# Optimization experiments

Hardware: AMD Instinct MI355X
Metric: run time of the kernel (lower is better)

## Reference

```python
import jax, jax.numpy as jnp
import numpy as np
import math

H = 16          # head_count
D = 1024        # model_dim
DT = 100        # topic_dim
DH = D // H     # dim_per_head


def _lin(x, W, b):
    return x @ W.T + b


def _shape(x, B):
    # [B, L, D] -> [B, H, L, DH]
    return x.reshape(B, -1, H, DH).transpose(0, 2, 1, 3)


def setup_inputs() -> dict:
    key = jax.random.key(0)
    ks = jax.random.split(key, 20)
    B, L = 4, 1024
    s = 0.02
    inp = {
        'key': jax.random.normal(ks[0], (B, L, D), jnp.float32),
        'value': jax.random.normal(ks[1], (B, L, D), jnp.float32),
        'query': jax.random.normal(ks[2], (B, L, D), jnp.float32),
        'mask': jax.random.randint(ks[3], (B, L, L), 0, 2).astype(bool),
        'topic_vec': jax.random.normal(ks[4], (B, L, DT), jnp.float32),
        'Wq': jax.random.normal(ks[5], (D, D), jnp.float32) * s,
        'bq': jnp.zeros((D,), jnp.float32),
        'Wk': jax.random.normal(ks[6], (D, D), jnp.float32) * s,
        'bk': jnp.zeros((D,), jnp.float32),
        'Wv': jax.random.normal(ks[7], (D, D), jnp.float32) * s,
        'bv': jnp.zeros((D,), jnp.float32),
        'Wtk': jax.random.normal(ks[8], (D, D), jnp.float32) * s,
        'btk': jnp.zeros((D,), jnp.float32),
        'Wtv': jax.random.normal(ks[9], (D, DT), jnp.float32) * s,
        'btv': jnp.zeros((D,), jnp.float32),
        'Wtw': jax.random.normal(ks[10], (H, 3 * D), jnp.float32) * s,
        'btw': jnp.zeros((H,), jnp.float32),
        'Wo': jax.random.normal(ks[11], (D, D), jnp.float32) * s,
        'bo': jnp.zeros((D,), jnp.float32),
    }
    return inp


def reference(key, value, query, mask, topic_vec,
              Wq, bq, Wk, bk, Wv, bv, Wtk, btk, Wtv, btv, Wtw, btw, Wo, bo):
    B = key.shape[0]
    # content and topic projections
    q_lin = _lin(query, Wq, bq)          # [B, L, D]
    k_lin = _lin(key, Wk, bk)
    v_lin = _lin(value, Wv, bv)
    tk_lin = _lin(key, Wtk, btk)         # topic keys from key states
    tv_lin = _lin(topic_vec, Wtv, btv)   # topic queries from topic distribution

    q = _shape(q_lin, B) / math.sqrt(DH)   # [B, H, Lq, DH]
    k = _shape(k_lin, B)
    v = _shape(v_lin, B)
    tk = _shape(tk_lin, B)
    tq = _shape(tv_lin, B) / math.sqrt(DH)

    scores = jnp.einsum('bhqd,bhkd->bhqk', q, k)          # content scores
    topic_scores = jnp.einsum('bhqd,bhkd->bhqk', tq, tk)  # topic scores

    # per-query, per-head mixing gate from concatenated projections (3*D -> H)
    gate = jax.nn.sigmoid(_lin(jnp.concatenate([q_lin, tk_lin, tv_lin], axis=-1), Wtw, btw))  # [B, L, H]
    p = gate.transpose(0, 2, 1)[..., None]                # [B, H, Lq, 1]
    scores = (1.0 - p) * scores + p * topic_scores

    # masked_fill(mask, -1e18), mask broadcast over heads
    scores = jnp.where(mask[:, None, :, :], -1e18, scores)
    attn = jax.nn.softmax(scores, axis=-1)
    # dropout is identity at eval time
    ctx = jnp.einsum('bhqk,bhkd->bhqd', attn, v)
    ctx = ctx.transpose(0, 2, 1, 3).reshape(B, -1, D)     # unshape
    return ctx @ Wo.T + bo
```

## Files before the change

kernel.cpp:

```cpp
#include <hip/hip_runtime.h>
#include <hip/hip_bf16.h>

#define BB 4
#define LL 1024
#define DD 1024
#define HH 16
#define DHH 64
#define DTT 100
#define ML (BB*LL)
#define LOG2E 1.4426950408889634f

typedef float f32x4 __attribute__((ext_vector_type(4)));
typedef short s16x8 __attribute__((ext_vector_type(8)));

__device__ __forceinline__ unsigned short f2bf(float x) {
    unsigned u = __builtin_bit_cast(unsigned, x);
    return (unsigned short)((u + 0x7FFFu + ((u >> 16) & 1u)) >> 16);
}
__device__ __forceinline__ unsigned short f2bf_fast(float x) {
    return (unsigned short)((__builtin_bit_cast(unsigned, x) + 0x8000u) >> 16);
}
__device__ __forceinline__ unsigned cvt_pk_bf16(float lo, float hi) {
    unsigned r;
    asm("v_cvt_pk_bf16_f32 %0, %1, %2" : "=v"(r) : "v"(lo), "v"(hi));
    return r;
}
__device__ __forceinline__ float bflo(unsigned u) { return __builtin_bit_cast(float, u << 16); }
__device__ __forceinline__ float bfhi(unsigned u) { return __builtin_bit_cast(float, u & 0xFFFF0000u); }
__device__ __forceinline__ int4 pack_bf16x8(float4 x0, float4 x1) {
    int4 o;
    o.x = cvt_pk_bf16(x0.x, x0.y); o.y = cvt_pk_bf16(x0.z, x0.w);
    o.z = cvt_pk_bf16(x1.x, x1.y); o.w = cvt_pk_bf16(x1.z, x1.w);
    return o;
}
__device__ __forceinline__ void gl_lds16(const unsigned short* g, char* l) {
    __builtin_amdgcn_global_load_lds(
        (const __attribute__((address_space(1))) unsigned*)g,
        (__attribute__((address_space(3))) unsigned*)l, 16, 0, 0);
}
__device__ __forceinline__ void barrier_lgkm() {
    __builtin_amdgcn_sched_barrier(0);
    asm volatile("s_waitcnt lgkmcnt(0)" ::: "memory");
    __builtin_amdgcn_sched_barrier(0);
    __builtin_amdgcn_s_barrier();
    __builtin_amdgcn_sched_barrier(0);
}

__global__ __launch_bounds__(256)
void conv_fused(const float* __restrict__ qf, const float* __restrict__ kf,
                const float* __restrict__ vf,
                unsigned short* __restrict__ qb, unsigned short* __restrict__ kb,
                unsigned short* __restrict__ vb,
                const float* __restrict__ w0, const float* __restrict__ w1,
                const float* __restrict__ w2, const float* __restrict__ w3,
                const float* __restrict__ w4, unsigned short* __restrict__ wd,
                const float* __restrict__ wtw, unsigned short* __restrict__ wtwd,
                const float* __restrict__ wtv, unsigned short* __restrict__ wtvd,
                const float* __restrict__ topic, unsigned short* __restrict__ topicd,
                const int* __restrict__ mask, unsigned long long* __restrict__ MB) {
    const int bx0 = blockIdx.x, tid = threadIdx.x;
    if (bx0 < 6144) {
        const int which = bx0 >> 11;
        const float* src = which == 0 ? qf : (which == 1 ? kf : vf);
        unsigned short* dst = which == 0 ? qb : (which == 1 ? kb : vb);
        const int idx = (bx0 & 2047) * 256 + tid;
        float4 f0 = *(const float4*)(src + (size_t)idx * 8);
        float4 f1 = *(const float4*)(src + (size_t)idx * 8 + 4);
        *(int4*)(dst + (size_t)idx * 8) = pack_bf16x8(f0, f1);
        return;
    }
    const int bx = bx0 - 6144;
    if (bx < 2560) {
        const int which = bx >> 9;
        const float* src;
        switch (which) {
            case 0:  src = w0; break;
            case 1:  src = w1; break;
            case 2:  src = w2; break;
            case 3:  src = w3; break;
            default: src = w4; break;
        }
        unsigned short* dst = wd + (size_t)which * DD * DD;
        const int idx = (bx & 511) * 256 + tid;
        float4 f0 = *(const float4*)(src + (size_t)idx * 8);
        float4 f1 = *(const float4*)(src + (size_t)idx * 8 + 4);
        *(int4*)(dst + (size_t)idx * 8) = pack_bf16x8(f0, f1);
    } else if (bx < 2584) {
        const int idx = (bx - 2560) * 256 + tid;
        float4 f0 = *(const float4*)(wtw + (size_t)idx * 8);
        float4 f1 = *(const float4*)(wtw + (size_t)idx * 8 + 4);
        *(int4*)(wtwd + (size_t)idx * 8) = pack_bf16x8(f0, f1);
    } else if (bx < 2648) {
        const int idx = (bx - 2584) * 256 + tid;
        const int r = idx >> 4, c0 = (idx & 15) * 8;
        unsigned short o[8];
        #pragma unroll
        for (int j = 0; j < 8; j++) {
            int c = c0 + j;
            o[j] = (c < DTT) ? f2bf(wtv[(size_t)r * DTT + c]) : (unsigned short)0;
        }
        int4 v;
        v.x = o[0] | ((unsigned)o[1] << 16);
        v.y = o[2] | ((unsigned)o[3] << 16);
        v.z = o[4] | ((unsigned)o[5] << 16);
        v.w = o[6] | ((unsigned)o[7] << 16);
        *(int4*)(wtvd + (size_t)r * 128 + c0) = v;
    } else if (bx < 2904) {
        const int idx = (bx - 2648) * 256 + tid;
        const int r = idx >> 4, c0 = (idx & 15) * 8;
        unsigned short o[8];
        #pragma unroll
        for (int j = 0; j < 8; j++) {
            int c = c0 + j;
            o[j] = (c < DTT) ? f2bf(topic[(size_t)r * DTT + c]) : (unsigned short)0;
        }
        int4 v;
        v.x = o[0] | ((unsigned)o[1] << 16);
        v.y = o[2] | ((unsigned)o[3] << 16);
        v.z = o[4] | ((unsigned)o[5] << 16);
        v.w = o[6] | ((unsigned)o[7] << 16);
        *(int4*)(topicd + (size_t)r * 128 + c0) = v;
    } else {
        const int ww = (bx - 2904) * 4 + (tid >> 6);
        const int lane = tid & 63;
        int v = mask[(size_t)ww * 64 + lane];
        unsigned long long bits = __ballot(v != 0);
        if (lane == 0) MB[ww] = bits;
    }
}

struct GArg { const void* A; const unsigned short* W; const float* bias; void* C; int mode; };

#define STAGE256(kt_, Ad_, Bd_) { \
    const unsigned short* agp_ = Ag + (size_t)(kt_) * 64; \
    const unsigned short* bgp_ = Bg + (size_t)(kt_) * 64; \
    _Pragma("unroll") \
    for (int i_ = 0; i_ < 4; i_++) { \
        gl_lds16(agp_ + (size_t)(i_ * 64) * K, (Ad_) + i_ * 8192 + ldst); \
        gl_lds16(bgp_ + (size_t)(i_ * 64) * K, (Bd_) + i_ * 8192 + ldst); \
    } }

__global__ __launch_bounds__(512, 2)
void gemm256(GArg a0, GArg a1, GArg a2, GArg a3, int N, int K) {
    __shared__ char lds[131072];

    const int nb = gridDim.x * gridDim.y * gridDim.z;
    const int flat = blockIdx.x + gridDim.x * (blockIdx.y + gridDim.y * blockIdx.z);
    const int wid = (flat & 7) * (nb >> 3) + (flat >> 3);
    const int bx = wid % gridDim.x;
    const int rem = wid / gridDim.x;
    const int by = rem % gridDim.y;
    const int bz = rem / gridDim.y;

    GArg a;
    switch (bz) {
        case 0:  a = a0; break;
        case 1:  a = a1; break;
        case 2:  a = a2; break;
        default: a = a3; break;
    }

    const int tid = threadIdx.x, w = tid >> 6, l = tid & 63;
    const int g = l >> 4, c = l & 15;
    const int wm = w >> 2, wn = w & 3;
    const int bm = by * 256, bn = bx * 256;
    const int NK = K >> 6;

    const int srow = tid >> 3;
    const int scol = (tid & 7) ^ (srow & 7);
    const unsigned short* const Ag = (const unsigned short*)a.A + (size_t)(bm + srow) * K + scol * 8;
    const unsigned short* const Bg = a.W + (size_t)(bn + srow) * K + scol * 8;
    const int ldst = tid * 16;

    f32x4 acc[8][4];
    #pragma unroll
    for (int m = 0; m < 8; m++)
        #pragma unroll
        for (int n = 0; n < 4; n++)
            #pragma unroll
            for (int j = 0; j < 4; j++) acc[m][n][j] = 0.f;

    STAGE256(0, lds, lds + 32768)
    if (NK > 1) STAGE256(1, lds + 65536, lds + 98304)

    for (int kt = 0; kt < NK; kt++) {
        char* Ab = lds + (kt & 1) * 65536;
        char* Bb = Ab + 32768;
        if (kt + 1 < NK) { asm volatile("s_waitcnt vmcnt(8)" ::: "memory"); }
        else             { asm volatile("s_waitcnt vmcnt(0)" ::: "memory"); }
        __builtin_amdgcn_sched_barrier(0);
        __builtin_amdgcn_s_barrier();
        __builtin_amdgcn_sched_barrier(0);

        s16x8 bfr[4][2];
        #pragma unroll
        for (int n = 0; n < 4; n++) {
            const int rb = wn * 64 + n * 16 + c;
            #pragma unroll
            for (int ks = 0; ks < 2; ks++)
                bfr[n][ks] = *(const s16x8*)(Bb + rb * 128 + (((ks * 4 + g) ^ (rb & 7)) << 4));
        }
        s16x8 a0[8];
        #pragma unroll
        for (int m = 0; m < 8; m++) {
            const int ra = wm * 128 + m * 16 + c;
            a0[m] = *(const s16x8*)(Ab + ra * 128 + ((g ^ (ra & 7)) << 4));
        }
        #pragma unroll
        for (int m = 0; m < 8; m++)
            #pragma unroll
            for (int n = 0; n < 4; n++)
                acc[m][n] = __builtin_amdgcn_mfma_f32_16x16x32_bf16(a0[m], bfr[n][0], acc[m][n], 0, 0, 0);
        s16x8 a1[8];
        #pragma unroll
        for (int m = 0; m < 8; m++) {
            const int ra = wm * 128 + m * 16 + c;
            a1[m] = *(const s16x8*)(Ab + ra * 128 + (((4 + g) ^ (ra & 7)) << 4));
        }
        barrier_lgkm();
        if (kt + 2 < NK) STAGE256(kt + 2, Ab, Bb)
        #pragma unroll
        for (int m = 0; m < 8; m++)
            #pragma unroll
            for (int n = 0; n < 4; n++)
                acc[m][n] = __builtin_amdgcn_mfma_f32_16x16x32_bf16(a1[m], bfr[n][1], acc[m][n], 0, 0, 0);
    }

    const int mode = a.mode;
    if (mode == 1) {
        unsigned short* C = (unsigned short*)a.C;
        #pragma unroll
        for (int n = 0; n < 4; n++) {
            const int col = bn + wn * 64 + n * 16 + c;
            const float bv = a.bias[col];
            #pragma unroll
            for (int m = 0; m < 8; m++) {
                const int row = bm + wm * 128 + m * 16 + g * 4;
                #pragma unroll
                for (int j = 0; j < 4; j++)
                    C[(size_t)(row + j) * N + col] = f2bf(acc[m][n][j] + bv);
            }
        }
    } else if (mode == 2 || mode == 3) {
        unsigned short* C = (unsigned short*)a.C;
        const int off = (mode == 2) ? 0 : 64;
        #pragma unroll
        for (int n = 0; n < 4; n++) {
            const int col = bn + wn * 64 + n * 16 + c;
            const float bv = a.bias[col];
            const int h = col >> 6, d = col & 63;
            #pragma unroll
            for (int m = 0; m < 8; m++) {
                const int row = bm + wm * 128 + m * 16 + g * 4;
                #pragma unroll
                for (int j = 0; j < 4; j++) {
                    const int rr = row + j;
                    C[((size_t)((rr >> 10) * HH + h) * LL + (rr & 1023)) * 128 + off + d] =
                        f2bf(acc[m][n][j] + bv);
                }
            }
        }
    } else {
        unsigned short* C = (unsigned short*)a.C;
        #pragma unroll
        for (int n = 0; n < 4; n++) {
            const int col = bn + wn * 64 + n * 16 + c;
            const float bv = a.bias[col];
            const int h = col >> 6, d = col & 63;
            #pragma unroll
            for (int m = 0; m < 8; m++) {
                const int row = bm + wm * 128 + m * 16 + g * 4;
                unsigned lo = cvt_pk_bf16(acc[m][n][0] + bv, acc[m][n][1] + bv);
                unsigned hi = cvt_pk_bf16(acc[m][n][2] + bv, acc[m][n][3] + bv);
                unsigned long long pk = (unsigned long long)lo | ((unsigned long long)hi << 32);
                *(unsigned long long*)(C + ((size_t)((row >> 10) * HH + h) * 64 + d) * LL + (row & 1023)) = pk;
            }
        }
    }
}

#define LOADW(s0_,s1_,s2_,s3_,kk) \
    s0_ = *(const int4*)(Wb + (kk)); \
    s1_ = *(const int4*)(Wb + (kk) + wstep); \
    s2_ = *(const int4*)(Wb + (kk) + 2 * wstep); \
    s3_ = *(const int4*)(Wb + (kk) + 3 * wstep);
#define STOREW(s0_,s1_,s2_,s3_) \
    *(int4*)(bsl)         = s0_; \
    *(int4*)(bsl + 4096)  = s1_; \
    *(int4*)(bsl + 8192)  = s2_; \
    *(int4*)(bsl + 12288) = s3_;
#define LOADA16(s0_,s1_,s2_,s3_,kk) \
    s0_ = *(const int4*)(Ab16 + (kk)); \
    s1_ = *(const int4*)(Ab16 + (kk) + wstep); \
    s2_ = *(const int4*)(Ab16 + (kk) + 2 * wstep); \
    s3_ = *(const int4*)(Ab16 + (kk) + 3 * wstep);
#define STOREA16(s0_,s1_,s2_,s3_) \
    *(int4*)(asl)         = s0_; \
    *(int4*)(asl + 4096)  = s1_; \
    *(int4*)(asl + 8192)  = s2_; \
    *(int4*)(asl + 12288) = s3_;
#define GEMM_COMPUTE(ABASE, BBASE) \
    _Pragma("unroll") \
    for (int ks = 0; ks < 2; ks++) { \
        s16x8 af[4], bf[4]; \
        _Pragma("unroll") \
        for (int m = 0; m < 4; m++) { \
            const int ra = wr * 64 + m * 16 + c; \
            af[m] = *(const s16x8*)((ABASE) + ra * 128 + (((ks * 4 + g) ^ (ra & 7)) << 4)); \
            const int rb = wc * 64 + m * 16 + c; \
            bf[m] = *(const s16x8*)((BBASE) + rb * 128 + (((ks * 4 + g) ^ (rb & 7)) << 4)); \
        } \
        _Pragma("unroll") \
        for (int m = 0; m < 4; m++) \
            _Pragma("unroll") \
            for (int n = 0; n < 4; n++) \
                acc[m][n] = __builtin_amdgcn_mfma_f32_16x16x32_bf16(af[m], bf[n], acc[m][n], 0, 0, 0); \
    }

__global__ __launch_bounds__(256, 3)
void gemm_mfma(GArg a0, GArg a1, GArg a2, GArg a3, int N, int K) {
    __shared__ char lds[32768];
    char* As = lds;
    char* Bs = lds + 16384;

    const int nb = gridDim.x * gridDim.y * gridDim.z;
    const int flat = blockIdx.x + gridDim.x * (blockIdx.y + gridDim.y * blockIdx.z);
    const int wid = (flat & 7) * (nb >> 3) + (flat >> 3);
    const int bx = wid % gridDim.x;
    const int rem = wid / gridDim.x;
    const int by = rem % gridDim.y;
    const int bz = rem / gridDim.y;

    GArg a;
    switch (bz) {
        case 0:  a = a0; break;
        case 1:  a = a1; break;
        case 2:  a = a2; break;
        default: a = a3; break;
    }

    const int tid = threadIdx.x, w = tid >> 6, l = tid & 63;
    const int g = l >> 4, c = l & 15;
    const int wr = w >> 1, wc = w & 1;
    const int bm = by * 128, bn = bx * 128;

    const int r0 = tid >> 3, sl = tid & 7;
    char* const asl = As + r0 * 128 + ((sl ^ (r0 & 7)) << 4);
    char* const bsl = Bs + r0 * 128 + ((sl ^ (r0 & 7)) << 4);
    const size_t wstep = (size_t)32 * K;
    const unsigned short* const Wb   = a.W + (size_t)(bn + r0) * K + sl * 8;
    const unsigned short* const Ab16 = (const unsigned short*)a.A + (size_t)(bm + r0) * K + sl * 8;

    f32x4 acc[4][4];
    #pragma unroll
    for (int m = 0; m < 4; m++)
        #pragma unroll
        for (int n = 0; n < 4; n++)
            #pragma unroll
            for (int j = 0; j < 4; j++) acc[m][n][j] = 0.f;

    int4 pw0, pw1, pw2, pw3;
    int4 pa0, pa1, pa2, pa3;
    LOADW(pw0, pw1, pw2, pw3, 0)
    LOADA16(pa0, pa1, pa2, pa3, 0)

    for (int k0 = 0; k0 < K; k0 += 64) {
        barrier_lgkm();
        STOREA16(pa0, pa1, pa2, pa3)
        STOREW(pw0, pw1, pw2, pw3)
        {
            const int kn = (k0 + 64 < K) ? (k0 + 64) : 0;
            LOADW(pw0, pw1, pw2, pw3, kn)
            LOADA16(pa0, pa1, pa2, pa3, kn)
        }
        barrier_lgkm();
        GEMM_COMPUTE(As, Bs)
    }

    const int mode = a.mode;
    if (mode == 0) {
        float* C = (float*)a.C;
        #pragma unroll
        for (int n = 0; n < 4; n++) {
            const int col = bn + wc * 64 + n * 16 + c;
            const float bv = a.bias[col];
            #pragma unroll
            for (int m = 0; m < 4; m++) {
                const int row = bm + wr * 64 + m * 16 + g * 4;
                #pragma unroll
                for (int j = 0; j < 4; j++)
                    C[(size_t)(row + j) * N + col] = acc[m][n][j] + bv;
            }
        }
    } else {
        unsigned short* C = (unsigned short*)a.C;
        #pragma unroll
        for (int n = 0; n < 4; n++) {
            const int col = bn + wc * 64 + n * 16 + c;
            const float bv = a.bias[col];
            #pragma unroll
            for (int m = 0; m < 4; m++) {
                const int row = bm + wr * 64 + m * 16 + g * 4;
                #pragma unroll
                for (int j = 0; j < 4; j++)
                    C[(size_t)(row + j) * N + col] = f2bf(acc[m][n][j] + bv);
            }
        }
    }
}

__global__ __launch_bounds__(256)
void gate_kernel(const unsigned short* __restrict__ QLb,
                 const unsigned short* __restrict__ KCb,
                 const unsigned short* __restrict__ TVLb,
                 const unsigned short* __restrict__ Wtwb,
                 const float* __restrict__ btw, float* __restrict__ GATE) {
    const int t = threadIdx.x;
    const int q = t >> 6, sub = t & 63, row = sub >> 4, h = sub & 15;
    const int row_g = blockIdx.x * 4 + row;
    const int b = row_g >> 10, l = row_g & 1023;

    float acc = 0.f;
    const unsigned short* wp = Wtwb + h * 3 * DD + q * 768;
    #pragma unroll 4
    for (int cc = 0; cc < 96; cc++) {
        const int i = q * 768 + cc * 8;
        const unsigned short* xp;
        if (i < 1024) {
            xp = QLb + (size_t)row_g * DD + i;
        } else if (i < 2048) {
            const int j = i - 1024;
            xp = KCb + ((size_t)(b * HH + (j >> 6)) * LL + l) * 128 + 64 + (j & 63);
        } else {
            xp = TVLb + (size_t)row_g * DD + (i - 2048);
        }
        int4 xv = *(const int4*)xp;
        int4 wv = *(const int4*)(wp + cc * 8);
        const unsigned xs[4] = {(unsigned)xv.x, (unsigned)xv.y, (unsigned)xv.z, (unsigned)xv.w};
        const unsigned ws[4] = {(unsigned)wv.x, (unsigned)wv.y, (unsigned)wv.z, (unsigned)wv.w};
        #pragma unroll
        for (int jj = 0; jj < 4; jj++) {
            acc = fmaf(bflo(xs[jj]), bflo(ws[jj]), acc);
            acc = fmaf(bfhi(xs[jj]), bfhi(ws[jj]), acc);
        }
    }
    __shared__ float part[4][4][16];
    part[q][row][h] = acc;
    __syncthreads();
    if (t < 64) {
        float s = part[0][row][h] + part[1][row][h] + part[2][row][h] + part[3][row][h] + btw[h];
        GATE[(size_t)row_g * HH + h] = 1.f / (1.f + __expf(-s));
    }
}

__global__ __launch_bounds__(256, 3)
void attn_mfma(const unsigned short* __restrict__ QLb,
               const unsigned short* __restrict__ TVLb,
               const float* __restrict__ GATE,
               const unsigned short* __restrict__ KC,
               const unsigned short* __restrict__ VT,
               const unsigned long long* __restrict__ MB,
               unsigned short* __restrict__ CTb) {
    __shared__ char lds[32768];
    char* kc_l = lds;
    char* vt_l = lds + 16384;
    char* p_l  = lds + 24576;

    const int tid = threadIdx.x, w = tid >> 6, l = tid & 63;
    const int g = l >> 4, c = l & 15;
    const int flat = blockIdx.y * gridDim.x + blockIdx.x;
    const int wid = (flat & 7) * 128 + (flat >> 3);
    const int qb = wid & 15, bh = wid >> 4;
    const int b = bh >> 4, h = bh & 15;
    const int q0 = qb * 64;

    const size_t kcg = (size_t)bh * LL * 128;
    const size_t vtg = (size_t)bh * 64 * LL;

    const int kr = tid >> 4, ks = tid & 15;
    const size_t kgo = (size_t)kr * 128 + ks * 8;
    char* const klb = kc_l + kr * 256 + ((ks ^ (kr & 7)) << 4);
    const int vr = tid >> 3, vs = tid & 7;
    const size_t vgo = (size_t)vr * LL + vs * 8;
    char* const vlb = vt_l + vr * 128 + ((vs ^ (vr & 7)) << 4);

    int4 pk0, pk1, pk2, pk3, pv0, pv1;
    {
        const unsigned short* kp = KC + kcg + kgo;
        pk0 = *(const int4*)kp;
        pk1 = *(const int4*)(kp + 16 * 128);
        pk2 = *(const int4*)(kp + 32 * 128);
        pk3 = *(const int4*)(kp + 48 * 128);
        const unsigned short* vp = VT + vtg + vgo;
        pv0 = *(const int4*)vp;
        pv1 = *(const int4*)(vp + 32 * LL);
    }

    {
        const size_t rowbase = (size_t)b * LL + q0 + kr;
        const unsigned short* qsrc =
            (ks < 8 ? QLb : TVLb) + rowbase * DD + h * DHH + (ks & 7) * 8;
        const float* gp = GATE + rowbase * HH + h;
        #pragma unroll
        for (int i = 0; i < 4; i++) {
            const float p = gp[(size_t)i * 16 * HH];
            const float sc = (ks < 8 ? 1.f - p : p) * (0.125f * LOG2E);
            int4 v = *(const int4*)(qsrc + (size_t)i * 16 * DD);
            int4 o;
            o.x = cvt_pk_bf16(bflo((unsigned)v.x) * sc, bfhi((unsigned)v.x) * sc);
            o.y = cvt_pk_bf16(bflo((unsigned)v.y) * sc, bfhi((unsigned)v.y) * sc);
            o.z = cvt_pk_bf16(bflo((unsigned)v.z) * sc, bfhi((unsigned)v.z) * sc);
            o.w = cvt_pk_bf16(bflo((unsigned)v.w) * sc, bfhi((unsigned)v.w) * sc);
            *(int4*)(klb + i * 4096) = o;
        }
    }
    barrier_lgkm();
    s16x8 qf[4];
    const int ql = w * 16 + c;
    #pragma unroll
    for (int kss = 0; kss < 4; kss++) {
        int t = kss * 4 + g;
        qf[kss] = *(s16x8*)(kc_l + ql * 256 + ((t ^ (ql & 7)) << 4));
    }

    f32x4 ctx[4], la;
    #pragma unroll
    for (int ct = 0; ct < 4; ct++)
        #pragma unroll
        for (int j = 0; j < 4; j++) ctx[ct][j] = 0.f;
    #pragma unroll
    for (int j = 0; j < 4; j++) la[j] = 0.f;
    float m_s = -1e18f;

    s16x8 ones;
    #pragma unroll
    for (int j = 0; j < 8; j++) ones[j] = (short)0x3F80;

    const unsigned long long* mbq = MB + ((size_t)b * LL + q0 + w * 16 + c) * 16;
    unsigned long long mw_cur = mbq[0];

    for (int kt = 0; kt < 16; kt++) {
        barrier_lgkm();
        *(int4*)(klb)          = pk0;
        *(int4*)(klb + 4096)   = pk1;
        *(int4*)(klb + 8192)   = pk2;
        *(int4*)(klb + 12288)  = pk3;
        *(int4*)(vlb)          = pv0;
        *(int4*)(vlb + 4096)   = pv1;
        unsigned long long mw_nxt;
        {
            const unsigned short* kp = KC + kcg + (size_t)(kt + 1) * (64 * 128) + kgo;
            pk0 = *(const int4*)kp;
            pk1 = *(const int4*)(kp + 16 * 128);
            pk2 = *(const int4*)(kp + 32 * 128);
            pk3 = *(const int4*)(kp + 48 * 128);
            const unsigned short* vp = VT + vtg + (size_t)(kt + 1) * 64 + vgo;
            pv0 = *(const int4*)vp;
            pv1 = *(const int4*)(vp + 32 * LL);
            mw_nxt = mbq[kt + 1 < 16 ? kt + 1 : 15];
        }
        barrier_lgkm();

        f32x4 sf[4];
        #pragma unroll
        for (int ct = 0; ct < 4; ct++) {
            f32x4 acc;
            #pragma unroll
            for (int j = 0; j < 4; j++) acc[j] = 0.f;
            const int rk = ct * 16 + c;
            #pragma unroll
            for (int kss = 0; kss < 4; kss++) {
                int t = kss * 4 + g;
                s16x8 kf = *(s16x8*)(kc_l + rk * 256 + ((t ^ (rk & 7)) << 4));
                acc = __builtin_amdgcn_mfma_f32_16x16x32_bf16(kf, qf[kss], acc, 0, 0, 0);
            }
            sf[ct] = acc;
        }

        {
            const unsigned long long mw = mw_cur;
            mw_cur = mw_nxt;
            const unsigned ms0 = (unsigned)(mw >> (g * 4));
            const unsigned ms1 = (unsigned)(mw >> (g * 4 + 32));
            #pragma unroll
            for (int ct = 0; ct < 4; ct++) {
                const unsigned mm = (ct & 2) ? ms1 : ms0;
                const int sh = (ct & 1) ? 16 : 0;
                #pragma unroll
                for (int j = 0; j < 4; j++)
                    if ((mm >> (sh + j)) & 1u) sf[ct][j] = -1e18f;
            }
            float t0 = fmaxf(fmaxf(sf[0][0], sf[0][1]), fmaxf(sf[0][2], sf[0][3]));
            float t1 = fmaxf(fmaxf(sf[1][0], sf[1][1]), fmaxf(sf[1][2], sf[1][3]));
            float t2 = fmaxf(fmaxf(sf[2][0], sf[2][1]), fmaxf(sf[2][2], sf[2][3]));
            float t3 = fmaxf(fmaxf(sf[3][0], sf[3][1]), fmaxf(sf[3][2], sf[3][3]));
            float mx = fmaxf(fmaxf(t0, t1), fmaxf(t2, t3));
            mx = fmaxf(mx, __shfl_xor(mx, 16));
            mx = fmaxf(mx, __shfl_xor(mx, 32));
            const float mn = fmaxf(m_s, mx);
            const float cf = exp2f(m_s - mn);
            m_s = mn;

            const float cr0 = __shfl(cf, g * 4 + 0, 16);
            const float cr1 = __shfl(cf, g * 4 + 1, 16);
            const float cr2 = __shfl(cf, g * 4 + 2, 16);
            const float cr3 = __shfl(cf, g * 4 + 3, 16);
            #pragma unroll
            for (int ct = 0; ct < 4; ct++) {
                ctx[ct][0] *= cr0; ctx[ct][1] *= cr1;
                ctx[ct][2] *= cr2; ctx[ct][3] *= cr3;
            }
            la[0] *= cr0; la[1] *= cr1; la[2] *= cr2; la[3] *= cr3;

            char* pw = p_l + w * 2048 + c * 128;
            #pragma unroll
            for (int ct = 0; ct < 4; ct++) {
                const unsigned lo = cvt_pk_bf16(exp2f(sf[ct][0] - mn), exp2f(sf[ct][1] - mn));
                const unsigned hi = cvt_pk_bf16(exp2f(sf[ct][2] - mn), exp2f(sf[ct][3] - mn));
                const unsigned long long pkv =
                    (unsigned long long)lo | ((unsigned long long)hi << 32);
                *(unsigned long long*)(pw + (((ct * 2 + (g >> 1)) ^ (c & 7)) << 4) + ((g & 1) << 3)) = pkv;
            }
        }

        char* pb = p_l + w * 2048;
        s16x8 pa0 = *(s16x8*)(pb + c * 128 + (((0 + g) ^ (c & 7)) << 4));
        s16x8 pa1 = *(s16x8*)(pb + c * 128 + (((4 + g) ^ (c & 7)) << 4));
        #pragma unroll
        for (int ct = 0; ct < 4; ct++) {
            const int dv = ct * 16 + c;
            s16x8 v0 = *(s16x8*)(vt_l + dv * 128 + (((0 + g) ^ (dv & 7)) << 4));
            s16x8 v1 = *(s16x8*)(vt_l + dv * 128 + (((4 + g) ^ (dv & 7)) << 4));
            ctx[ct] = __builtin_amdgcn_mfma_f32_16x16x32_bf16(pa0, v0, ctx[ct], 0, 0, 0);
            ctx[ct] = __builtin_amdgcn_mfma_f32_16x16x32_bf16(pa1, v1, ctx[ct], 0, 0, 0);
        }
        la = __builtin_amdgcn_mfma_f32_16x16x32_bf16(pa0, ones, la, 0, 0, 0);
        la = __builtin_amdgcn_mfma_f32_16x16x32_bf16(pa1, ones, la, 0, 0, 0);
    }

    #pragma unroll
    for (int r = 0; r < 4; r++) {
        const float inv = 1.f / la[r];
        const int q = q0 + w * 16 + g * 4 + r;
        unsigned short* dst = CTb + ((size_t)b * LL + q) * DD + h * DHH + c;
        dst[0]  = f2bf(ctx[0][r] * inv);
        dst[16] = f2bf(ctx[1][r] * inv);
        dst[32] = f2bf(ctx[2][r] * inv);
        dst[48] = f2bf(ctx[3][r] * inv);
    }
}

extern "C" void kernel_launch(void* const* d_in, const int* in_sizes, int n_in,
                              void* d_out, int out_size, void* d_ws, size_t ws_size,
                              hipStream_t stream) {
    const float* key   = (const float*)d_in[0];
    const float* value = (const float*)d_in[1];
    const float* query = (const float*)d_in[2];
    const int*   mask  = (const int*)d_in[3];
    const float* topic = (const float*)d_in[4];
    const float* Wq  = (const float*)d_in[5];  const float* bq  = (const float*)d_in[6];
    const float* Wk  = (const float*)d_in[7];  const float* bk  = (const float*)d_in[8];
    const float* Wv  = (const float*)d_in[9];  const float* bv  = (const float*)d_in[10];
    const float* Wtk = (const float*)d_in[11]; const float* btk = (const float*)d_in[12];
    const float* Wtv = (const float*)d_in[13]; const float* btv = (const float*)d_in[14];
    const float* Wtw = (const float*)d_in[15]; const float* btw = (const float*)d_in[16];
    const float* Wo  = (const float*)d_in[17]; const float* bo  = (const float*)d_in[18];
    float* out = (float*)d_out;

    const size_t NTOK = (size_t)ML * DD;
    unsigned short* Wqb   = (unsigned short*)d_ws;
    unsigned short* Wkb   = Wqb  + (size_t)DD * DD;
    unsigned short* Wvb   = Wkb  + (size_t)DD * DD;
    unsigned short* Wtkb  = Wvb  + (size_t)DD * DD;
    unsigned short* Wob   = Wtkb + (size_t)DD * DD;
    unsigned short* Wtvb  = Wob  + (size_t)DD * DD;
    unsigned short* Wtwb  = Wtvb + (size_t)DD * 128;
    unsigned short* topicb= Wtwb + (size_t)HH * 3 * DD;
    unsigned short* QLb   = topicb + (size_t)ML * 128;
    unsigned short* TVLb  = QLb  + NTOK;
    unsigned short* CTb   = TVLb + NTOK;
    unsigned short* KCb   = CTb  + NTOK;
    unsigned short* VTb   = KCb  + (size_t)BB * HH * LL * 128;
    float* GATE           = (float*)(VTb + (size_t)BB * HH * 64 * LL);
    unsigned long long* MBp = (unsigned long long*)(GATE + (size_t)ML * HH);
    unsigned short* QBb   = (unsigned short*)(MBp + (size_t)BB * LL * LL / 64);
    unsigned short* KBb   = QBb + NTOK;
    unsigned short* VBb   = KBb + NTOK;

    conv_fused<<<25432, 256, 0, stream>>>(query, key, value, QBb, KBb, VBb,
                                          Wq, Wk, Wv, Wtk, Wo, Wqb,
                                          Wtw, Wtwb, Wtv, Wtvb, topic, topicb,
                                          mask, MBp);

    gemm256<<<dim3(DD / 256, ML / 256, 4), 512, 0, stream>>>(
        GArg{QBb, Wqb,  bq,  QLb, 1},
        GArg{KBb, Wkb,  bk,  KCb, 2},
        GArg{VBb, Wvb,  bv,  VTb, 4},
        GArg{KBb, Wtkb, btk, KCb, 3},
        DD, DD);
    gemm_mfma<<<dim3(DD / 128, ML / 128, 1), 256, 0, stream>>>(
        GArg{topicb, Wtvb, btv, TVLb, 1},
        GArg{topicb, Wtvb, btv, TVLb, 1},
        GArg{topicb, Wtvb, btv, TVLb, 1},
        GArg{topicb, Wtvb, btv, TVLb, 1},
        DD, 128);

    gate_kernel<<<ML / 4, 256, 0, stream>>>(QLb, KCb, TVLb, Wtwb, btw, GATE);

    attn_mfma<<<dim3(LL / 64, BB * HH), 256, 0, stream>>>(QLb, TVLb, GATE, KCb, VTb, MBp, CTb);

    gemm_mfma<<<dim3(DD / 128, ML / 128, 1), 256, 0, stream>>>(
        GArg{CTb, Wob, bo, out, 0},
        GArg{CTb, Wob, bo, out, 0},
        GArg{CTb, Wob, bo, out, 0},
        GArg{CTb, Wob, bo, out, 0},
        DD, DD);
}
```

Measured before the change: 199.9 us.

## Fold topic projection into batched gemm256, add MFMA priority, simplify attn sync

The topic-vector projection GEMM (K=128) becomes a fifth z-slice of the batched gemm256 launch, with a per-argument K, which removes one kernel launch. MFMA blocks in gemm256 are wrapped in s_setprio raises so compute waves get issue priority over loads. In the attention kernel the LDS-count barriers become full __syncthreads, and the mask-word prefetch is replaced by a direct load each iteration. The K=128 slice runs only two k-steps on 256x256 tiles, so those blocks are short and may balance poorly against the K=1024 slices.

```diff
diff --git a/kernel.cpp b/kernel.cpp
--- a/kernel.cpp
+++ b/kernel.cpp
@@ -129,7 +129,7 @@
     }
 }
 
-struct GArg { const void* A; const unsigned short* W; const float* bias; void* C; int mode; };
+struct GArg { const void* A; const unsigned short* W; const float* bias; void* C; int mode; int K; };
 
 #define STAGE256(kt_, Ad_, Bd_) { \
     const unsigned short* agp_ = Ag + (size_t)(kt_) * 64; \
@@ -141,7 +141,7 @@
     } }
 
 __global__ __launch_bounds__(512, 2)
-void gemm256(GArg a0, GArg a1, GArg a2, GArg a3, int N, int K) {
+void gemm256(GArg a0, GArg a1, GArg a2, GArg a3, GArg a4, int N) {
     __shared__ char lds[131072];
 
     const int nb = gridDim.x * gridDim.y * gridDim.z;
@@ -157,8 +157,10 @@
         case 0:  a = a0; break;
         case 1:  a = a1; break;
         case 2:  a = a2; break;
-        default: a = a3; break;
-    }
+        case 3:  a = a3; break;
+        default: a = a4; break;
+    }
+    const int K = a.K;
 
     const int tid = threadIdx.x, w = tid >> 6, l = tid & 63;
     const int g = l >> 4, c = l & 15;
@@ -206,11 +208,13 @@
             const int ra = wm * 128 + m * 16 + c;
             a0[m] = *(const s16x8*)(Ab + ra * 128 + ((g ^ (ra & 7)) << 4));
         }
+        __builtin_amdgcn_s_setprio(1);
         #pragma unroll
         for (int m = 0; m < 8; m++)
             #pragma unroll
             for (int n = 0; n < 4; n++)
                 acc[m][n] = __builtin_amdgcn_mfma_f32_16x16x32_bf16(a0[m], bfr[n][0], acc[m][n], 0, 0, 0);
+        __builtin_amdgcn_s_setprio(0);
         s16x8 a1[8];
         #pragma unroll
         for (int m = 0; m < 8; m++) {
@@ -219,11 +223,13 @@
         }
         barrier_lgkm();
         if (kt + 2 < NK) STAGE256(kt + 2, Ab, Bb)
+        __builtin_amdgcn_s_setprio(1);
         #pragma unroll
         for (int m = 0; m < 8; m++)
             #pragma unroll
             for (int n = 0; n < 4; n++)
                 acc[m][n] = __builtin_amdgcn_mfma_f32_16x16x32_bf16(a1[m], bfr[n][1], acc[m][n], 0, 0, 0);
+        __builtin_amdgcn_s_setprio(0);
     }
 
     const int mode = a.mode;
@@ -514,7 +520,7 @@
             *(int4*)(klb + i * 4096) = o;
         }
     }
-    barrier_lgkm();
+    __syncthreads();
     s16x8 qf[4];
     const int ql = w * 16 + c;
     #pragma unroll
@@ -537,17 +543,15 @@
     for (int j = 0; j < 8; j++) ones[j] = (short)0x3F80;
 
     const unsigned long long* mbq = MB + ((size_t)b * LL + q0 + w * 16 + c) * 16;
-    unsigned long long mw_cur = mbq[0];
 
     for (int kt = 0; kt < 16; kt++) {
-        barrier_lgkm();
+        __syncthreads();
         *(int4*)(klb)          = pk0;
         *(int4*)(klb + 4096)   = pk1;
         *(int4*)(klb + 8192)   = pk2;
         *(int4*)(klb + 12288)  = pk3;
         *(int4*)(vlb)          = pv0;
         *(int4*)(vlb + 4096)   = pv1;
-        unsigned long long mw_nxt;
         {
             const unsigned short* kp = KC + kcg + (size_t)(kt + 1) * (64 * 128) + kgo;
             pk0 = *(const int4*)kp;
@@ -557,9 +561,8 @@
             const unsigned short* vp = VT + vtg + (size_t)(kt + 1) * 64 + vgo;
             pv0 = *(const int4*)vp;
             pv1 = *(const int4*)(vp + 32 * LL);
-            mw_nxt = mbq[kt + 1 < 16 ? kt + 1 : 15];
-        }
-        barrier_lgkm();
+        }
+        __syncthreads();
 
         f32x4 sf[4];
         #pragma unroll
@@ -578,8 +581,7 @@
         }
 
         {
-            const unsigned long long mw = mw_cur;
-            mw_cur = mw_nxt;
+            const unsigned long long mw = mbq[kt];
             const unsigned ms0 = (unsigned)(mw >> (g * 4));
             const unsigned ms1 = (unsigned)(mw >> (g * 4 + 32));
             #pragma unroll
@@ -692,27 +694,22 @@
                                           Wtw, Wtwb, Wtv, Wtvb, topic, topicb,
                                           mask, MBp);
 
-    gemm256<<<dim3(DD / 256, ML / 256, 4), 512, 0, stream>>>(
-        GArg{QBb, Wqb,  bq,  QLb, 1},
-        GArg{KBb, Wkb,  bk,  KCb, 2},
-        GArg{VBb, Wvb,  bv,  VTb, 4},
-        GArg{KBb, Wtkb, btk, KCb, 3},
+    gemm256<<<dim3(DD / 256, ML / 256, 5), 512, 0, stream>>>(
+        GArg{QBb,    Wqb,  bq,  QLb,  1, DD},
+        GArg{KBb,    Wkb,  bk,  KCb,  2, DD},
+        GArg{VBb,    Wvb,  bv,  VTb,  4, DD},
+        GArg{KBb,    Wtkb, btk, KCb,  3, DD},
+        GArg{topicb, Wtvb, btv, TVLb, 1, 128},
+        DD);
+
+    gate_kernel<<<ML / 4, 256, 0, stream>>>(QLb, KCb, TVLb, Wtwb, btw, GATE);
+
+    attn_mfma<<<dim3(LL / 64, BB * HH), 256, 0, stream>>>(QLb, TVLb, GATE, KCb, VTb, MBp, CTb);
+
+    gemm_mfma<<<dim3(DD / 128, ML / 128, 1), 256, 0, stream>>>(
+        GArg{CTb, Wob, bo, out, 0, DD},
+        GArg{CTb, Wob, bo, out, 0, DD},
+        GArg{CTb, Wob, bo, out, 0, DD},
+        GArg{CTb, Wob, bo, out, 0, DD},
         DD, DD);
-    gemm_mfma<<<dim3(DD / 128, ML / 128, 1), 256, 0, stream>>>(
-        GArg{topicb, Wtvb, btv, TVLb, 1},
-        GArg{topicb, Wtvb, btv, TVLb, 1},
-        GArg{topicb, Wtvb, btv, TVLb, 1},
-        GArg{topicb, Wtvb, btv, TVLb, 1},
-        DD, 128);
-
-    gate_kernel<<<ML / 4, 256, 0, stream>>>(QLb, KCb, TVLb, Wtwb, btw, GATE);
-
-    attn_mfma<<<dim3(LL / 64, BB * HH), 256, 0, stream>>>(QLb, TVLb, GATE, KCb, VTb, MBp, CTb);
-
-    gemm_mfma<<<dim3(DD / 128, ML / 128, 1), 256, 0, stream>>>(
-        GArg{CTb, Wob, bo, out, 0},
-        GArg{CTb, Wob, bo, out, 0},
-        GArg{CTb, Wob, bo, out, 0},
-        GArg{CTb, Wob, bo, out, 0},
-        DD, DD);
-}
+}
```

New measurement: 216.5 us. 1.08x slower.
